# Kernel optimization log

Hardware: AMD Instinct MI355X
Metric: run time of the kernel (lower is better)

Reference implementation:

```python
import jax, jax.numpy as jnp
import numpy as np
import math

D_MODEL = 1024
NUM_HEADS = 16
D_K = D_MODEL // NUM_HEADS


def setup_inputs() -> dict:
    key = jax.random.key(0)
    ks = jax.random.split(key, 9)
    s = 1.0 / math.sqrt(D_MODEL)
    x = jax.random.normal(ks[0], (2, 2048, D_MODEL), dtype=jnp.float32)
    # torch Linear params: weight [out, in], bias [out]
    Wq = jax.random.uniform(ks[1], (D_MODEL, D_MODEL), jnp.float32, -s, s)
    bq = jax.random.uniform(ks[2], (D_MODEL,), jnp.float32, -s, s)
    Wk = jax.random.uniform(ks[3], (D_MODEL, D_MODEL), jnp.float32, -s, s)
    bk = jax.random.uniform(ks[4], (D_MODEL,), jnp.float32, -s, s)
    Wv = jax.random.uniform(ks[5], (D_MODEL, D_MODEL), jnp.float32, -s, s)
    bv = jax.random.uniform(ks[6], (D_MODEL,), jnp.float32, -s, s)
    Wo = jax.random.uniform(ks[7], (D_MODEL, D_MODEL), jnp.float32, -s, s)
    bo = jax.random.uniform(ks[8], (D_MODEL,), jnp.float32, -s, s)
    return {"x": x, "Wq": Wq, "bq": bq, "Wk": Wk, "bk": bk,
            "Wv": Wv, "bv": bv, "Wo": Wo, "bo": bo}


def reference(x, Wq, bq, Wk, bk, Wv, bv, Wo, bo):
    B, T, _ = x.shape
    scale = 1.0 / math.sqrt(D_MODEL)  # NOTE: module scales by sqrt(d_model), not sqrt(d_k)

    def proj(W, b):
        # torch Linear: x @ W^T + b, then split heads -> [B, H, T, d_k]
        y = jnp.einsum('btd,ed->bte', x, W) + b
        return y.reshape(B, T, NUM_HEADS, D_K).transpose(0, 2, 1, 3)

    Q = proj(Wq, bq)
    K = proj(Wk, bk)
    V = proj(Wv, bv)
    logits = jnp.einsum('bhtd,bhsd->bhts', Q, K) * scale  # [B,H,T,T]
    attn = jax.nn.softmax(logits, axis=-1)
    out = jnp.einsum('bhts,bhsd->bhtd', attn, V)  # [B,H,T,d_k]
    out = out.transpose(0, 2, 1, 3).reshape(B, T, D_MODEL)
    return jnp.einsum('btd,ed->bte', out, Wo) + bo
```

## Files before the change

kernel.cpp:

```cpp
#include <hip/hip_runtime.h>

#define T_SEQ 2048
#define NB 2
#define NH 16
#define DK 64
#define DMODEL 1024

typedef __bf16 bf16x8 __attribute__((ext_vector_type(8)));
typedef float f32x4 __attribute__((ext_vector_type(4)));
typedef unsigned short ushortx8 __attribute__((ext_vector_type(8)));
typedef unsigned short ushortx4 __attribute__((ext_vector_type(4)));

__device__ inline unsigned short f2b1(float f) {
  unsigned u = __float_as_uint(f);
  u += 0x7fffu + ((u >> 16) & 1u);
  return (unsigned short)(u >> 16);
}

__device__ inline void gload16(const void* g, void* l) {
  __builtin_amdgcn_global_load_lds((const __attribute__((address_space(1))) void*)g,
                                   (__attribute__((address_space(3))) void*)l, 16, 0, 0);
}

__device__ inline bf16x8 mk8(unsigned a, unsigned b, unsigned c, unsigned d) {
  uint4 t = {a, b, c, d};
  return *(bf16x8*)&t;
}

__global__ void prep(const float* __restrict__ x,
                     const float* __restrict__ w0, const float* __restrict__ w1,
                     const float* __restrict__ w2, const float* __restrict__ w3,
                     const float* __restrict__ bq, const float* __restrict__ bk,
                     const float* __restrict__ bv,
                     unsigned short* __restrict__ xb, unsigned short* __restrict__ Wqkv,
                     float* __restrict__ bqkv) {
  int bid = blockIdx.x, tid = threadIdx.x;
  if (bid < 4096) {
    int i = (bid * 256 + tid) * 4;
    float4 v = *(const float4*)(x + i);
    ushortx4 o;
    o.x = f2b1(v.x); o.y = f2b1(v.y); o.z = f2b1(v.z); o.w = f2b1(v.w);
    *(ushortx4*)(xb + i) = o;
  } else if (bid < 8192) {
    int which = (bid - 4096) >> 10;
    int i = (((bid - 4096) & 1023) * 256 + tid) * 4;
    const float* src = which == 0 ? w0 : which == 1 ? w1 : which == 2 ? w2 : w3;
    float4 v = *(const float4*)(src + i);
    ushortx4 o;
    o.x = f2b1(v.x); o.y = f2b1(v.y); o.z = f2b1(v.z); o.w = f2b1(v.w);
    *(ushortx4*)(Wqkv + (long)which * 1048576 + i) = o;
  } else {
    int i = (bid - 8192) * 256 + tid;
    if (i < 3072) {
      float v = (i < 1024) ? bq[i] : (i < 2048 ? bk[i - 1024] : bv[i - 2048]);
      bqkv[i] = v;
    }
  }
}

__global__ __launch_bounds__(256, 3)
void gemm_qkv(const unsigned short* __restrict__ A, const unsigned short* __restrict__ B,
              const float* __restrict__ bias, unsigned short* __restrict__ Cb,
              unsigned short* __restrict__ Vt, int M, int N, int K, float scl) {
  __shared__ unsigned short As[2][4096];
  __shared__ unsigned short Bs[2][4096];
  const int tid = threadIdx.x;
  const int w = tid >> 6, lane = tid & 63;
  const int quad = lane >> 4, l16 = lane & 15;
  const int bm = blockIdx.y, bn = blockIdx.x;
  const int wm = w >> 1, wn = w & 1;

  f32x4 acc[4][4] = {};

  const int srow = tid >> 2;
  const int c4 = tid & 3;
  const unsigned short* aG = A + (long)(bm * 128 + srow) * K + c4 * 8;
  const unsigned short* bG = B + (long)(bn * 128 + srow) * K + c4 * 8;
  const long rs64 = (long)64 * K;
  const int wo = w * 512;

  gload16(aG, As[0] + wo);
  gload16(aG + rs64, As[0] + 2048 + wo);
  gload16(bG, Bs[0] + wo);
  gload16(bG + rs64, Bs[0] + 2048 + wo);

  int buf = 0;
  for (int kt = 0; kt < K; kt += 32) {
    __syncthreads();
    {
      const int nb = buf ^ 1;
      gload16(aG + kt + 32, As[nb] + wo);
      gload16(aG + rs64 + kt + 32, As[nb] + 2048 + wo);
      gload16(bG + kt + 32, Bs[nb] + wo);
      gload16(bG + rs64 + kt + 32, Bs[nb] + 2048 + wo);
    }

    bf16x8 af[4], bfr[4];
#pragma unroll
    for (int mt = 0; mt < 4; mt++)
      af[mt] = *(const bf16x8*)(As[buf] + (wm * 64 + mt * 16 + l16) * 32 + quad * 8);
#pragma unroll
    for (int nt = 0; nt < 4; nt++)
      bfr[nt] = *(const bf16x8*)(Bs[buf] + (wn * 64 + nt * 16 + l16) * 32 + quad * 8);
#pragma unroll
    for (int mt = 0; mt < 4; mt++)
#pragma unroll
      for (int nt = 0; nt < 4; nt++)
        acc[mt][nt] = __builtin_amdgcn_mfma_f32_16x16x32_bf16(af[mt], bfr[nt], acc[mt][nt], 0, 0, 0);
    buf ^= 1;
  }

  const int col0 = bn * 128 + wn * 64 + l16;
  const bool isV = (bn * 128) >= 2048;
#pragma unroll
  for (int mt = 0; mt < 4; mt++) {
    int row0 = bm * 128 + wm * 64 + mt * 16 + quad * 4;
#pragma unroll
    for (int nt = 0; nt < 4; nt++) {
      int col = col0 + nt * 16;
      float bb = bias[col];
      float s = (col < 1024) ? scl : 1.0f;
      if (!isV) {
#pragma unroll
        for (int r = 0; r < 4; r++)
          Cb[(long)(row0 + r) * N + col] = f2b1((acc[mt][nt][r] + bb) * s);
      } else {
        int cv = col - 2048;
        int h = cv >> 6, d = cv & 63;
        int b = row0 >> 11, t0 = row0 & 2047;
        ushortx4 o;
        o.x = f2b1(acc[mt][nt][0] + bb);
        o.y = f2b1(acc[mt][nt][1] + bb);
        o.z = f2b1(acc[mt][nt][2] + bb);
        o.w = f2b1(acc[mt][nt][3] + bb);
        *(ushortx4*)(Vt + ((long)((b * NH + h) * DK + d)) * T_SEQ + t0) = o;
      }
    }
  }
}

__global__ __launch_bounds__(256, 2)
void gemm_out(const unsigned short* __restrict__ A, const unsigned short* __restrict__ B,
              const float* __restrict__ bias, float* __restrict__ Cf, int M, int N, int K) {
  __shared__ unsigned short As[2][2048];
  __shared__ unsigned short Bs[2][4096];
  const int tid = threadIdx.x;
  const int w = tid >> 6, lane = tid & 63;
  const int quad = lane >> 4, l16 = lane & 15;
  const int bm = blockIdx.y, bn = blockIdx.x;
  const int wm = w >> 1, wn = w & 1;

  f32x4 acc[2][4] = {};

  const int srow = tid >> 2;
  const int c4 = tid & 3;
  const unsigned short* aG = A + (long)(bm * 64 + srow) * K + c4 * 8;
  const unsigned short* bG = B + (long)(bn * 128 + srow) * K + c4 * 8;
  const long rs64 = (long)64 * K;
  const int wo = w * 512;

  gload16(aG, As[0] + wo);
  gload16(bG, Bs[0] + wo);
  gload16(bG + rs64, Bs[0] + 2048 + wo);

  int buf = 0;
  for (int kt = 0; kt < K; kt += 32) {
    __syncthreads();
    {
      const int nb = buf ^ 1;
      gload16(aG + kt + 32, As[nb] + wo);
      gload16(bG + kt + 32, Bs[nb] + wo);
      gload16(bG + rs64 + kt + 32, Bs[nb] + 2048 + wo);
    }

    bf16x8 af[2], bfr[4];
#pragma unroll
    for (int mt = 0; mt < 2; mt++)
      af[mt] = *(const bf16x8*)(As[buf] + (wm * 32 + mt * 16 + l16) * 32 + quad * 8);
#pragma unroll
    for (int nt = 0; nt < 4; nt++)
      bfr[nt] = *(const bf16x8*)(Bs[buf] + (wn * 64 + nt * 16 + l16) * 32 + quad * 8);
#pragma unroll
    for (int mt = 0; mt < 2; mt++)
#pragma unroll
      for (int nt = 0; nt < 4; nt++)
        acc[mt][nt] = __builtin_amdgcn_mfma_f32_16x16x32_bf16(af[mt], bfr[nt], acc[mt][nt], 0, 0, 0);
    buf ^= 1;
  }

  const int col0 = bn * 128 + wn * 64 + l16;
#pragma unroll
  for (int mt = 0; mt < 2; mt++) {
    int row0 = bm * 64 + wm * 32 + mt * 16 + quad * 4;
#pragma unroll
    for (int nt = 0; nt < 4; nt++) {
      int col = col0 + nt * 16;
      float bb = bias[col];
#pragma unroll
      for (int r = 0; r < 4; r++)
        Cf[(long)(row0 + r) * N + col] = acc[mt][nt][r] + bb;
    }
  }
}

__global__ __launch_bounds__(256, 4)
void attn3(const unsigned short* __restrict__ QKV, const unsigned short* __restrict__ Vt,
           unsigned short* __restrict__ Onum, float* __restrict__ Oden) {
  __shared__ unsigned short Ks[2][4096];
  __shared__ unsigned short Vs[2][4096];
  const int tid = threadIdx.x;
  const int w = tid >> 6, lane = tid & 63;
  const int quad = lane >> 4, l16 = lane & 15;

  const int id = blockIdx.x;
  const int group = (id & 7) | (((id >> 3) & 7) << 3);
  const int qt = id >> 6;
  const int bh = group >> 1, split = group & 1;
  const int b = bh >> 4, h = bh & 15;
  const long qkvBase = (long)b * T_SEQ * 3072;
  const int kv0 = split * 1024;

  bf16x8 qf[2][2];
#pragma unroll
  for (int g = 0; g < 2; g++) {
    const unsigned short* qp = QKV + qkvBase + (long)(qt * 128 + w * 32 + g * 16 + l16) * 3072 + h * 64 + quad * 8;
    qf[g][0] = *(const bf16x8*)qp;
    qf[g][1] = *(const bf16x8*)(qp + 32);
  }

  const unsigned short* kG[2];
  const unsigned short* vG[2];
#pragma unroll
  for (int i = 0; i < 2; i++) {
    int S = w * 128 + i * 64 + lane;
    int row = S >> 3;
    int c = (S & 7) ^ (row & 7);
    kG[i] = QKV + qkvBase + 1024 + h * 64 + (long)(kv0 + row) * 3072 + c * 8;
    vG[i] = Vt + (long)bh * DK * T_SEQ + (long)row * T_SEQ + kv0 + c * 8;
  }
  const int wo2 = w * 1024;

  gload16(kG[0], Ks[0] + wo2);
  gload16(kG[1], Ks[0] + wo2 + 512);
  gload16(vG[0], Vs[0] + wo2);
  gload16(vG[1], Vs[0] + wo2 + 512);
  kG[0] += 64 * 3072; kG[1] += 64 * 3072;
  vG[0] += 64;        vG[1] += 64;

  f32x4 acco[2][4] = {};
  float psum[2] = {0.f, 0.f};
  int buf = 0;
  const int e16 = (l16 & 7) * 16;

  for (int it = 0; it < 16; it++) {
    __syncthreads();
    {
      const int nb = buf ^ 1;
      gload16(kG[0], Ks[nb] + wo2);
      gload16(kG[1], Ks[nb] + wo2 + 512);
      gload16(vG[0], Vs[nb] + wo2);
      gload16(vG[1], Vs[nb] + wo2 + 512);
      kG[0] += 64 * 3072; kG[1] += 64 * 3072;
      vG[0] += 64;        vG[1] += 64;
    }

    f32x4 st[2][4];
#pragma unroll
    for (int nt = 0; nt < 4; nt++) {
      const char* kr = (char*)(Ks[buf]) + (nt * 16 + l16) * 128;
      bf16x8 k0 = *(const bf16x8*)(kr + ((quad * 16) ^ e16));
      bf16x8 k1 = *(const bf16x8*)(kr + (((quad + 4) * 16) ^ e16));
#pragma unroll
      for (int g = 0; g < 2; g++) {
        f32x4 z = {};
        z = __builtin_amdgcn_mfma_f32_16x16x32_bf16(k0, qf[g][0], z, 0, 0, 0);
        z = __builtin_amdgcn_mfma_f32_16x16x32_bf16(k1, qf[g][1], z, 0, 0, 0);
        st[g][nt] = z;
      }
    }

    bf16x8 pa[2][2];
#pragma unroll
    for (int g = 0; g < 2; g++) {
      unsigned pk[4][2];
#pragma unroll
      for (int nt = 0; nt < 4; nt++) {
        float p0 = __builtin_amdgcn_exp2f(st[g][nt][0]);
        float p1 = __builtin_amdgcn_exp2f(st[g][nt][1]);
        float p2 = __builtin_amdgcn_exp2f(st[g][nt][2]);
        float p3 = __builtin_amdgcn_exp2f(st[g][nt][3]);
        psum[g] += (p0 + p1) + (p2 + p3);
        unsigned a0 = __float_as_uint(p0) + 0x8000u;
        unsigned a1 = __float_as_uint(p1) + 0x8000u;
        unsigned a2 = __float_as_uint(p2) + 0x8000u;
        unsigned a3 = __float_as_uint(p3) + 0x8000u;
        pk[nt][0] = __builtin_amdgcn_perm(a1, a0, 0x07060302u);
        pk[nt][1] = __builtin_amdgcn_perm(a3, a2, 0x07060302u);
      }
      pa[g][0] = mk8(pk[0][0], pk[0][1], pk[1][0], pk[1][1]);
      pa[g][1] = mk8(pk[2][0], pk[2][1], pk[3][0], pk[3][1]);
    }

    const int off8 = (quad & 1) * 8;
    const int cq = quad >> 1;
#pragma unroll
    for (int nt = 0; nt < 4; nt++) {
      const char* vr = (char*)(Vs[buf]) + (nt * 16 + l16) * 128;
#pragma unroll
      for (int km = 0; km < 2; km++) {
        uint2 lo = *(const uint2*)(vr + (((km * 4 + cq) * 16) ^ e16) + off8);
        uint2 hi = *(const uint2*)(vr + (((km * 4 + cq + 2) * 16) ^ e16) + off8);
        bf16x8 vf = mk8(lo.x, lo.y, hi.x, hi.y);
#pragma unroll
        for (int g = 0; g < 2; g++)
          acco[g][nt] = __builtin_amdgcn_mfma_f32_16x16x32_bf16(pa[g][km], vf, acco[g][nt], 0, 0, 0);
      }
    }
    buf ^= 1;
  }

  const long rowBase = (long)bh * T_SEQ + qt * 128 + w * 32;
  const long numBase = ((long)split * 65536 + rowBase) * 64;
#pragma unroll
  for (int g = 0; g < 2; g++) {
    float v = psum[g];
    v += __shfl_xor(v, 16, 64);
    v += __shfl_xor(v, 32, 64);
    if (lane < 16)
      Oden[(long)split * 65536 + rowBase + g * 16 + lane] = v;
#pragma unroll
    for (int nt = 0; nt < 4; nt++)
#pragma unroll
      for (int r = 0; r < 4; r++)
        Onum[numBase + (long)(g * 16 + quad * 4 + r) * 64 + nt * 16 + l16] = f2b1(acco[g][nt][r]);
  }
}

__global__ __launch_bounds__(256)
void combine(const unsigned short* __restrict__ Onum, const float* __restrict__ Oden,
             unsigned short* __restrict__ Ob) {
  int idx = blockIdx.x * 256 + threadIdx.x;
  int rp = idx >> 4;
  int dq = (idx & 15) * 4;
  ushortx4 n0 = *(const ushortx4*)(Onum + (long)rp * 64 + dq);
  ushortx4 n1 = *(const ushortx4*)(Onum + 4194304L + (long)rp * 64 + dq);
  float den = Oden[rp] + Oden[65536 + rp];
  float rl = __builtin_amdgcn_rcpf(den);
  int bh = rp >> 11, t = rp & 2047;
  int b = bh >> 4, h = bh & 15;
  ushortx4 o;
  o.x = f2b1((__uint_as_float((unsigned)n0.x << 16) + __uint_as_float((unsigned)n1.x << 16)) * rl);
  o.y = f2b1((__uint_as_float((unsigned)n0.y << 16) + __uint_as_float((unsigned)n1.y << 16)) * rl);
  o.z = f2b1((__uint_as_float((unsigned)n0.z << 16) + __uint_as_float((unsigned)n1.z << 16)) * rl);
  o.w = f2b1((__uint_as_float((unsigned)n0.w << 16) + __uint_as_float((unsigned)n1.w << 16)) * rl);
  *(ushortx4*)(Ob + (long)(b * T_SEQ + t) * DMODEL + h * 64 + dq) = o;
}

extern "C" void kernel_launch(void* const* d_in, const int* in_sizes, int n_in,
                              void* d_out, int out_size, void* d_ws, size_t ws_size,
                              hipStream_t stream) {
  const float* x  = (const float*)d_in[0];
  const float* Wq = (const float*)d_in[1];
  const float* bq = (const float*)d_in[2];
  const float* Wk = (const float*)d_in[3];
  const float* bk = (const float*)d_in[4];
  const float* Wv = (const float*)d_in[5];
  const float* bv = (const float*)d_in[6];
  const float* Wo = (const float*)d_in[7];
  const float* bo = (const float*)d_in[8];
  float* out = (float*)d_out;

  unsigned short* xb   = (unsigned short*)d_ws;
  unsigned short* Wqkv = xb + 4194304;
  unsigned short* Wob  = Wqkv + 3145728;
  float*          bqkv = (float*)(Wob + 1048576);
  unsigned short* QKV  = (unsigned short*)(bqkv + 3072);
  unsigned short* Vt   = QKV + 12582912;
  unsigned short* Ob   = Vt + 4194304;
  unsigned short* Onum = Ob + 4194304;
  float*          Oden = (float*)(Onum + 8388608);

  prep<<<8204, 256, 0, stream>>>(x, Wq, Wk, Wv, Wo, bq, bk, bv, xb, Wqkv, bqkv);

  gemm_qkv<<<dim3(24, 32), 256, 0, stream>>>(xb, Wqkv, bqkv, QKV, Vt,
                                             4096, 3072, 1024, 0.04508422037f);

  attn3<<<dim3(1024), 256, 0, stream>>>(QKV, Vt, Onum, Oden);
  combine<<<dim3(4096), 256, 0, stream>>>(Onum, Oden, Ob);

  gemm_out<<<dim3(8, 64), 256, 0, stream>>>(Ob, Wob, bo, out, 4096, 1024, 1024);
}
```

Measured before the change: 195.2 us.

## Halve attention query tile, drop LDS double buffering, raise occupancy

Result: slower. 218.8 us (+12.1%).

```diff
diff --git a/kernel.cpp b/kernel.cpp
--- a/kernel.cpp
+++ b/kernel.cpp
@@ -203,30 +203,26 @@
   }
 }
 
-__global__ __launch_bounds__(256, 4)
-void attn3(const unsigned short* __restrict__ QKV, const unsigned short* __restrict__ Vt,
+__global__ __launch_bounds__(256, 8)
+void attn4(const unsigned short* __restrict__ QKV, const unsigned short* __restrict__ Vt,
            unsigned short* __restrict__ Onum, float* __restrict__ Oden) {
-  __shared__ unsigned short Ks[2][4096];
-  __shared__ unsigned short Vs[2][4096];
+  __shared__ unsigned short Ks[4096];
+  __shared__ unsigned short Vs[4096];
   const int tid = threadIdx.x;
   const int w = tid >> 6, lane = tid & 63;
   const int quad = lane >> 4, l16 = lane & 15;
 
   const int id = blockIdx.x;
-  const int group = (id & 7) | (((id >> 3) & 7) << 3);
+  const int g64 = id & 63;
   const int qt = id >> 6;
-  const int bh = group >> 1, split = group & 1;
+  const int bh = g64 >> 1, split = g64 & 1;
   const int b = bh >> 4, h = bh & 15;
   const long qkvBase = (long)b * T_SEQ * 3072;
   const int kv0 = split * 1024;
 
-  bf16x8 qf[2][2];
-#pragma unroll
-  for (int g = 0; g < 2; g++) {
-    const unsigned short* qp = QKV + qkvBase + (long)(qt * 128 + w * 32 + g * 16 + l16) * 3072 + h * 64 + quad * 8;
-    qf[g][0] = *(const bf16x8*)qp;
-    qf[g][1] = *(const bf16x8*)(qp + 32);
-  }
+  const unsigned short* qp = QKV + qkvBase + (long)(qt * 64 + w * 16 + l16) * 3072 + h * 64 + quad * 8;
+  bf16x8 qf0 = *(const bf16x8*)qp;
+  bf16x8 qf1 = *(const bf16x8*)(qp + 32);
 
   const unsigned short* kG[2];
   const unsigned short* vG[2];
@@ -240,100 +236,77 @@
   }
   const int wo2 = w * 1024;
 
-  gload16(kG[0], Ks[0] + wo2);
-  gload16(kG[1], Ks[0] + wo2 + 512);
-  gload16(vG[0], Vs[0] + wo2);
-  gload16(vG[1], Vs[0] + wo2 + 512);
-  kG[0] += 64 * 3072; kG[1] += 64 * 3072;
-  vG[0] += 64;        vG[1] += 64;
-
-  f32x4 acco[2][4] = {};
-  float psum[2] = {0.f, 0.f};
-  int buf = 0;
+  f32x4 acco[4] = {};
+  float psum = 0.f;
   const int e16 = (l16 & 7) * 16;
 
   for (int it = 0; it < 16; it++) {
     __syncthreads();
-    {
-      const int nb = buf ^ 1;
-      gload16(kG[0], Ks[nb] + wo2);
-      gload16(kG[1], Ks[nb] + wo2 + 512);
-      gload16(vG[0], Vs[nb] + wo2);
-      gload16(vG[1], Vs[nb] + wo2 + 512);
-      kG[0] += 64 * 3072; kG[1] += 64 * 3072;
-      vG[0] += 64;        vG[1] += 64;
-    }
-
-    f32x4 st[2][4];
-#pragma unroll
-    for (int nt = 0; nt < 4; nt++) {
-      const char* kr = (char*)(Ks[buf]) + (nt * 16 + l16) * 128;
+    gload16(kG[0], Ks + wo2);
+    gload16(kG[1], Ks + wo2 + 512);
+    gload16(vG[0], Vs + wo2);
+    gload16(vG[1], Vs + wo2 + 512);
+    kG[0] += 64 * 3072; kG[1] += 64 * 3072;
+    vG[0] += 64;        vG[1] += 64;
+    __syncthreads();
+
+    f32x4 st[4];
+#pragma unroll
+    for (int nt = 0; nt < 4; nt++) {
+      const char* kr = (char*)Ks + (nt * 16 + l16) * 128;
       bf16x8 k0 = *(const bf16x8*)(kr + ((quad * 16) ^ e16));
       bf16x8 k1 = *(const bf16x8*)(kr + (((quad + 4) * 16) ^ e16));
-#pragma unroll
-      for (int g = 0; g < 2; g++) {
-        f32x4 z = {};
-        z = __builtin_amdgcn_mfma_f32_16x16x32_bf16(k0, qf[g][0], z, 0, 0, 0);
-        z = __builtin_amdgcn_mfma_f32_16x16x32_bf16(k1, qf[g][1], z, 0, 0, 0);
-        st[g][nt] = z;
-      }
-    }
-
-    bf16x8 pa[2][2];
-#pragma unroll
-    for (int g = 0; g < 2; g++) {
-      unsigned pk[4][2];
-#pragma unroll
-      for (int nt = 0; nt < 4; nt++) {
-        float p0 = __builtin_amdgcn_exp2f(st[g][nt][0]);
-        float p1 = __builtin_amdgcn_exp2f(st[g][nt][1]);
-        float p2 = __builtin_amdgcn_exp2f(st[g][nt][2]);
-        float p3 = __builtin_amdgcn_exp2f(st[g][nt][3]);
-        psum[g] += (p0 + p1) + (p2 + p3);
-        unsigned a0 = __float_as_uint(p0) + 0x8000u;
-        unsigned a1 = __float_as_uint(p1) + 0x8000u;
-        unsigned a2 = __float_as_uint(p2) + 0x8000u;
-        unsigned a3 = __float_as_uint(p3) + 0x8000u;
-        pk[nt][0] = __builtin_amdgcn_perm(a1, a0, 0x07060302u);
-        pk[nt][1] = __builtin_amdgcn_perm(a3, a2, 0x07060302u);
-      }
-      pa[g][0] = mk8(pk[0][0], pk[0][1], pk[1][0], pk[1][1]);
-      pa[g][1] = mk8(pk[2][0], pk[2][1], pk[3][0], pk[3][1]);
-    }
+      f32x4 z = {};
+      z = __builtin_amdgcn_mfma_f32_16x16x32_bf16(k0, qf0, z, 0, 0, 0);
+      z = __builtin_amdgcn_mfma_f32_16x16x32_bf16(k1, qf1, z, 0, 0, 0);
+      st[nt] = z;
+    }
+
+    unsigned pk[4][2];
+#pragma unroll
+    for (int nt = 0; nt < 4; nt++) {
+      float p0 = __builtin_amdgcn_exp2f(st[nt][0]);
+      float p1 = __builtin_amdgcn_exp2f(st[nt][1]);
+      float p2 = __builtin_amdgcn_exp2f(st[nt][2]);
+      float p3 = __builtin_amdgcn_exp2f(st[nt][3]);
+      psum += (p0 + p1) + (p2 + p3);
+      unsigned a0 = __float_as_uint(p0) + 0x8000u;
+      unsigned a1 = __float_as_uint(p1) + 0x8000u;
+      unsigned a2 = __float_as_uint(p2) + 0x8000u;
+      unsigned a3 = __float_as_uint(p3) + 0x8000u;
+      pk[nt][0] = __builtin_amdgcn_perm(a1, a0, 0x07060302u);
+      pk[nt][1] = __builtin_amdgcn_perm(a3, a2, 0x07060302u);
+    }
+    bf16x8 pa0 = mk8(pk[0][0], pk[0][1], pk[1][0], pk[1][1]);
+    bf16x8 pa1 = mk8(pk[2][0], pk[2][1], pk[3][0], pk[3][1]);
 
     const int off8 = (quad & 1) * 8;
     const int cq = quad >> 1;
 #pragma unroll
     for (int nt = 0; nt < 4; nt++) {
-      const char* vr = (char*)(Vs[buf]) + (nt * 16 + l16) * 128;
+      const char* vr = (char*)Vs + (nt * 16 + l16) * 128;
 #pragma unroll
       for (int km = 0; km < 2; km++) {
         uint2 lo = *(const uint2*)(vr + (((km * 4 + cq) * 16) ^ e16) + off8);
         uint2 hi = *(const uint2*)(vr + (((km * 4 + cq + 2) * 16) ^ e16) + off8);
         bf16x8 vf = mk8(lo.x, lo.y, hi.x, hi.y);
-#pragma unroll
-        for (int g = 0; g < 2; g++)
-          acco[g][nt] = __builtin_amdgcn_mfma_f32_16x16x32_bf16(pa[g][km], vf, acco[g][nt], 0, 0, 0);
+        acco[nt] = __builtin_amdgcn_mfma_f32_16x16x32_bf16(km == 0 ? pa0 : pa1, vf, acco[nt], 0, 0, 0);
       }
     }
-    buf ^= 1;
-  }
-
-  const long rowBase = (long)bh * T_SEQ + qt * 128 + w * 32;
+  }
+
+  const long rowBase = (long)bh * T_SEQ + qt * 64 + w * 16;
   const long numBase = ((long)split * 65536 + rowBase) * 64;
-#pragma unroll
-  for (int g = 0; g < 2; g++) {
-    float v = psum[g];
-    v += __shfl_xor(v, 16, 64);
-    v += __shfl_xor(v, 32, 64);
-    if (lane < 16)
-      Oden[(long)split * 65536 + rowBase + g * 16 + lane] = v;
-#pragma unroll
-    for (int nt = 0; nt < 4; nt++)
-#pragma unroll
-      for (int r = 0; r < 4; r++)
-        Onum[numBase + (long)(g * 16 + quad * 4 + r) * 64 + nt * 16 + l16] = f2b1(acco[g][nt][r]);
-  }
+  float v = psum;
+  v += __shfl_xor(v, 16, 64);
+  v += __shfl_xor(v, 32, 64);
+  if (lane < 16)
+    Oden[(long)split * 65536 + rowBase + lane] = v;
+#pragma unroll
+  for (int nt = 0; nt < 4; nt++)
+#pragma unroll
+    for (int r = 0; r < 4; r++)
+      Onum[numBase + (long)(quad * 4 + r) * 64 + nt * 16 + l16] = f2b1(acco[nt][r]);
 }
 
 __global__ __launch_bounds__(256)
@@ -385,7 +358,7 @@
   gemm_qkv<<<dim3(24, 32), 256, 0, stream>>>(xb, Wqkv, bqkv, QKV, Vt,
                                              4096, 3072, 1024, 0.04508422037f);
 
-  attn3<<<dim3(1024), 256, 0, stream>>>(QKV, Vt, Onum, Oden);
+  attn4<<<dim3(2048), 256, 0, stream>>>(QKV, Vt, Onum, Oden);
   combine<<<dim3(4096), 256, 0, stream>>>(Onum, Oden, Ob);
 
   gemm_out<<<dim3(8, 64), 256, 0, stream>>>(Ob, Wob, bo, out, 4096, 1024, 1024);
```
